# Kernel optimization log

Hardware: AMD Instinct MI355X
Metric: run time of the kernel (lower is better)

Reference implementation:

```python
import jax, jax.numpy as jnp
import numpy as np

D_MODEL = 1024
NUM_HEADS = 16
THETA = 10000.0
B, T = 2, 2048


def _rope(x, pos, theta_base):
    # x: (b, h, t, d_h); interleaved pairs (x0,x1),(x2,x3),... per the
    # rearrange '... (c d) -> ... c d' with d=2 in the original module.
    d = x.shape[-1]
    half = d // 2
    inv_freq = 1.0 / (theta_base ** (2.0 * jnp.arange(half, dtype=jnp.float32) / d))
    ang = pos.astype(jnp.float32)[:, None] * inv_freq[None, :]  # (t, half)
    sin = jnp.sin(ang)[None, None]  # (1,1,t,half)
    cos = jnp.cos(ang)[None, None]
    x1 = x[..., 0::2]
    x2 = x[..., 1::2]
    r1 = x1 * cos - x2 * sin
    r2 = x1 * sin + x2 * cos
    return jnp.stack([r1, r2], axis=-1).reshape(x.shape)


def setup_inputs() -> dict:
    key = jax.random.key(0)
    k0, k1, k2, k3, k4 = jax.random.split(key, 5)
    sigma = (2.0 / (D_MODEL + D_MODEL)) ** 0.5
    return {
        "in_features": jax.random.normal(k0, (B, T, D_MODEL), dtype=jnp.float32),
        "Wq": jax.random.normal(k1, (D_MODEL, D_MODEL), dtype=jnp.float32) * sigma,
        "Wk": jax.random.normal(k2, (D_MODEL, D_MODEL), dtype=jnp.float32) * sigma,
        "Wv": jax.random.normal(k3, (D_MODEL, D_MODEL), dtype=jnp.float32) * sigma,
        "Wo": jax.random.normal(k4, (D_MODEL, D_MODEL), dtype=jnp.float32) * sigma,
        "token_positions": jnp.arange(T, dtype=jnp.int32),
    }


def reference(in_features, Wq, Wk, Wv, Wo, token_positions):
    b, t, d_model = in_features.shape
    h = NUM_HEADS
    d_h = d_model // h
    # Fused-style QKV projections (x @ W.T, weights stored (in, out))
    q = in_features @ Wq.T
    k = in_features @ Wk.T
    v = in_features @ Wv.T
    # (b, t, h*d_h) -> (b, h, t, d_h)
    q = q.reshape(b, t, h, d_h).transpose(0, 2, 1, 3)
    k = k.reshape(b, t, h, d_h).transpose(0, 2, 1, 3)
    v = v.reshape(b, t, h, d_h).transpose(0, 2, 1, 3)
    q = _rope(q, token_positions, THETA)
    k = _rope(k, token_positions, THETA)
    scale = 1.0 / jnp.sqrt(jnp.asarray(d_h, dtype=q.dtype))
    scores = jnp.einsum('bhqd,bhkd->bhqk', q, k) * scale
    causal = jnp.tril(jnp.ones((t, t), dtype=bool))
    scores = jnp.where(causal[None, None], scores, -jnp.inf)
    attn = jax.nn.softmax(scores, axis=-1)
    out = jnp.einsum('bhqk,bhkd->bhqd', attn, v)
    out = out.transpose(0, 2, 1, 3).reshape(b, t, h * d_h)
    return out @ Wo.T
```

## Files before the change

kernel.cpp:

```cpp
#include <hip/hip_runtime.h>

#define D_MODEL 1024
#define NUM_HEADS 16
#define DH 64
#define B_SZ 2
#define T_SZ 2048
#define M_ROWS (B_SZ * T_SZ)

typedef __bf16 bf16;
typedef __bf16 bf16x4 __attribute__((ext_vector_type(4)));
typedef __bf16 bf16x8 __attribute__((ext_vector_type(8)));
typedef float f32x4 __attribute__((ext_vector_type(4)));

__device__ __forceinline__ void async_copy16(const bf16* g, bf16* l) {
  __builtin_amdgcn_global_load_lds(
      (const __attribute__((address_space(1))) void*)g,
      (__attribute__((address_space(3))) void*)l, 16, 0, 0);
}

#define NX (M_ROWS * D_MODEL / 4)
#define NW (D_MODEL * D_MODEL / 4)

__global__ __launch_bounds__(256) void cast_all(
    const float* __restrict__ X, const float* __restrict__ Wq,
    const float* __restrict__ Wk, const float* __restrict__ Wv,
    const float* __restrict__ Wo,
    bf16* __restrict__ Xb, bf16* __restrict__ Wqb, bf16* __restrict__ Wkb,
    bf16* __restrict__ Wvb, bf16* __restrict__ Wob) {
  int i = blockIdx.x * 256 + threadIdx.x;
  const float* s; bf16* d; int off;
  if (i < NX) {
    s = X; d = Xb; off = i;
  } else {
    int j = i - NX;
    int w = j >> 18;
    off = j & (NW - 1);
    if (w == 0)      { s = Wq; d = Wqb; }
    else if (w == 1) { s = Wk; d = Wkb; }
    else if (w == 2) { s = Wv; d = Wvb; }
    else             { s = Wo; d = Wob; }
  }
  float4 v = ((const float4*)s)[off];
  bf16x4 o;
  o[0] = (bf16)v.x; o[1] = (bf16)v.y; o[2] = (bf16)v.z; o[3] = (bf16)v.w;
  ((bf16x4*)d)[off] = o;
}

__global__ __launch_bounds__(256) void qkv_gemm(
    const bf16* __restrict__ Xb,
    const bf16* __restrict__ Wqb, const bf16* __restrict__ Wkb,
    const bf16* __restrict__ Wvb,
    bf16* __restrict__ Q, bf16* __restrict__ K, bf16* __restrict__ V) {
  __shared__ bf16 As[128 * 32];
  __shared__ bf16 Bs[128 * 32];

  int tid = threadIdx.x;
  int wave = tid >> 6, lane = tid & 63;
  int wm = wave >> 1, wn = wave & 1;
  int l15 = lane & 15, quad = lane >> 4;

  int row0 = blockIdx.x * 128;
  int col0 = blockIdx.y * 128;
  int sel = col0 >> 10;
  int nb = col0 & 1023;
  const bf16* W; bf16* Out;
  if (sel == 0)      { W = Wqb; Out = Q; }
  else if (sel == 1) { W = Wkb; Out = K; }
  else               { W = Wvb; Out = V; }

  int srow = tid >> 2;
  int schunk = tid & 3;
  const bf16* Ag = Xb + (size_t)(row0 + srow) * D_MODEL + schunk * 8;
  const bf16* Bg = W + (size_t)(nb + srow) * D_MODEL + schunk * 8;
  bf16* Al0 = &As[srow * 32 + schunk * 8];
  bf16* Al1 = &As[(srow + 64) * 32 + schunk * 8];
  bf16* Bl0 = &Bs[srow * 32 + schunk * 8];
  bf16* Bl1 = &Bs[(srow + 64) * 32 + schunk * 8];

  f32x4 acc[4][4];
#pragma unroll
  for (int i = 0; i < 4; ++i)
#pragma unroll
    for (int j = 0; j < 4; ++j) acc[i][j] = (f32x4){0.f, 0.f, 0.f, 0.f};

  for (int k0 = 0; k0 < D_MODEL; k0 += 32) {
    async_copy16(Ag + k0, Al0);
    async_copy16(Ag + k0 + (size_t)64 * D_MODEL, Al1);
    async_copy16(Bg + k0, Bl0);
    async_copy16(Bg + k0 + (size_t)64 * D_MODEL, Bl1);
    __syncthreads();

    bf16x8 af[4], bfr[4];
#pragma unroll
    for (int i = 0; i < 4; ++i)
      af[i] = *(const bf16x8*)&As[(wm * 64 + i * 16 + l15) * 32 + quad * 8];
#pragma unroll
    for (int j = 0; j < 4; ++j)
      bfr[j] = *(const bf16x8*)&Bs[(wn * 64 + j * 16 + l15) * 32 + quad * 8];
#pragma unroll
    for (int i = 0; i < 4; ++i)
#pragma unroll
      for (int j = 0; j < 4; ++j)
        acc[i][j] = __builtin_amdgcn_mfma_f32_16x16x32_bf16(af[i], bfr[j],
                                                            acc[i][j], 0, 0, 0);
    __syncthreads();
  }

#pragma unroll
  for (int i = 0; i < 4; ++i) {
    int row = row0 + wm * 64 + i * 16 + quad * 4;
#pragma unroll
    for (int j = 0; j < 4; ++j) {
      int col = nb + wn * 64 + j * 16 + l15;
#pragma unroll
      for (int r = 0; r < 4; ++r)
        Out[(size_t)(row + r) * D_MODEL + col] = (bf16)acc[i][j][r];
    }
  }
}

#define ROPEK_BLOCKS (M_ROWS * NUM_HEADS * 32 / 256)

__global__ __launch_bounds__(256) void ropek_vt(
    bf16* __restrict__ K, const bf16* __restrict__ V, bf16* __restrict__ VT,
    const int* __restrict__ pos) {
  int b0 = blockIdx.x;
  if (b0 < ROPEK_BLOCKS) {
    int idx = b0 * 256 + threadIdx.x;
    int i = idx & 31;
    int h = (idx >> 5) & 15;
    int row = idx >> 9;
    int t = row & (T_SZ - 1);
    float p = (float)pos[t];
    float freq = __expf(-(float)i * 0.28782313662425f);
    float s, c;
    sincosf(p * freq, &s, &c);
    size_t base = (size_t)row * D_MODEL + h * DH + 2 * i;
    float k1 = (float)K[base], k2 = (float)K[base + 1];
    K[base]     = (bf16)(k1 * c - k2 * s);
    K[base + 1] = (bf16)(k1 * s + k2 * c);
  } else {
    __shared__ bf16 tile[64][72];
    int vb = b0 - ROPEK_BLOCKS;
    int bh = vb >> 5;
    int tt = vb & 31;
    int b = bh >> 4, h = bh & 15;
    int tid = threadIdx.x;
    int rr = tid >> 3;
    int cc = (tid & 7) * 8;
#pragma unroll
    for (int p = 0; p < 2; ++p) {
      int t = rr + p * 32;
      bf16x8 v = *(const bf16x8*)&V[((size_t)b * T_SZ + tt * 64 + t) * D_MODEL +
                                    h * DH + cc];
      *(bf16x8*)&tile[t][cc] = v;
    }
    __syncthreads();
#pragma unroll
    for (int p = 0; p < 2; ++p) {
      int d = rr + p * 32;
      bf16x8 o;
#pragma unroll
      for (int j = 0; j < 8; ++j) o[j] = tile[cc + j][d];
      *(bf16x8*)&VT[((size_t)bh * DH + d) * T_SZ + tt * 64 + cc] = o;
    }
  }
}

#define PST 72

__global__ __launch_bounds__(512) void attn_kernel(
    const bf16* __restrict__ Q, const bf16* __restrict__ K,
    const bf16* __restrict__ VT, const int* __restrict__ pos,
    bf16* __restrict__ AO) {
  __shared__ bf16 Kt0[64 * 32], Kt1[64 * 32];
  __shared__ bf16 Vt0[64 * 32], Vt1[64 * 32];
  __shared__ bf16 Pbuf[8][16 * PST];

  int bh = blockIdx.x;
  int qi = 15 - (int)blockIdx.y;
  int bb = bh >> 4, h = bh & 15;
  int tid = threadIdx.x;
  int wave = tid >> 6, lane = tid & 63;
  int l15 = lane & 15, quad = lane >> 4;

  int q0 = qi * 128 + wave * 16;
  size_t grow = (size_t)bb * T_SZ + q0;

  const bf16* Qp = Q + (grow + l15) * D_MODEL + h * DH + quad * 8;
  bf16x8 bq0 = *(const bf16x8*)(Qp);
  bf16x8 bq1 = *(const bf16x8*)(Qp + 32);
  {
    float p = (float)pos[q0 + l15];
#pragma unroll
    for (int jj = 0; jj < 4; ++jj) {
      int i0 = quad * 4 + jj;
      float s, c;
      sincosf(p * __expf(-(float)i0 * 0.28782313662425f), &s, &c);
      float x1 = (float)bq0[2 * jj], x2 = (float)bq0[2 * jj + 1];
      bq0[2 * jj]     = (bf16)(x1 * c - x2 * s);
      bq0[2 * jj + 1] = (bf16)(x1 * s + x2 * c);
      sincosf(p * __expf(-(float)(i0 + 16) * 0.28782313662425f), &s, &c);
      float y1 = (float)bq1[2 * jj], y2 = (float)bq1[2 * jj + 1];
      bq1[2 * jj]     = (bf16)(y1 * c - y2 * s);
      bq1[2 * jj + 1] = (bf16)(y1 * s + y2 * c);
    }
  }

  f32x4 o[4];
#pragma unroll
  for (int nt = 0; nt < 4; ++nt) o[nt] = (f32x4){0.f, 0.f, 0.f, 0.f};
  float l_i = 0.f;

  bool isK = (tid < 256);
  int stid = isK ? tid : tid - 256;
  int srow = stid >> 2, sch = stid & 3;
  const bf16* sbase = isK
      ? K + ((size_t)bb * T_SZ + srow) * D_MODEL + h * DH + sch * 8
      : VT + ((size_t)bh * DH + srow) * T_SZ + sch * 8;
  size_t sstep = isK ? (size_t)64 * D_MODEL : (size_t)64;
  bf16* sdst0 = isK ? &Kt0[srow * 32 + sch * 8] : &Vt0[srow * 32 + sch * 8];
  bf16* sdst1 = isK ? &Kt1[srow * 32 + sch * 8] : &Vt1[srow * 32 + sch * 8];

  bf16* Pw = Pbuf[wave];
  int nchunks = 2 * qi + 2;
  int tb = 2 * qi + (wave >> 2);
  int bound = (wave & 3) * 16 + l15;

  for (int t = 0; t < nchunks; ++t) {
    const bf16* s = sbase + (size_t)t * sstep;
    async_copy16(s, sdst0);
    async_copy16(s + 32, sdst1);
    __syncthreads();

    if (t <= tb) {
      f32x4 st[4];
#pragma unroll
      for (int cs = 0; cs < 4; ++cs) {
        bf16x8 ak0 = *(const bf16x8*)&Kt0[(cs * 16 + l15) * 32 + quad * 8];
        bf16x8 ak1 = *(const bf16x8*)&Kt1[(cs * 16 + l15) * 32 + quad * 8];
        f32x4 s4 = (f32x4){0.f, 0.f, 0.f, 0.f};
        s4 = __builtin_amdgcn_mfma_f32_16x16x32_bf16(ak0, bq0, s4, 0, 0, 0);
        s4 = __builtin_amdgcn_mfma_f32_16x16x32_bf16(ak1, bq1, s4, 0, 0, 0);
        st[cs] = s4;
      }

      bool bm = (t == tb);
      float ps = 0.f;
#pragma unroll
      for (int cs = 0; cs < 4; ++cs)
#pragma unroll
        for (int r = 0; r < 4; ++r) {
          float p = __expf(st[cs][r] * 0.125f);
          if (bm) {
            int cl = cs * 16 + quad * 4 + r;
            p = (cl > bound) ? 0.f : p;
          }
          st[cs][r] = p;
          ps += p;
        }
      l_i += ps;

#pragma unroll
      for (int cs = 0; cs < 4; ++cs) {
        bf16x4 pk;
#pragma unroll
        for (int r = 0; r < 4; ++r) pk[r] = (bf16)st[cs][r];
        *(bf16x4*)&Pw[l15 * PST + cs * 16 + quad * 4] = pk;
      }
      __asm__ __volatile__("" ::: "memory");
      bf16x8 bp0 = *(const bf16x8*)&Pw[l15 * PST + quad * 8];
      bf16x8 bp1 = *(const bf16x8*)&Pw[l15 * PST + 32 + quad * 8];
      __asm__ __volatile__("" ::: "memory");

#pragma unroll
      for (int nt = 0; nt < 4; ++nt) {
        bf16x8 av0 = *(const bf16x8*)&Vt0[(nt * 16 + l15) * 32 + quad * 8];
        bf16x8 av1 = *(const bf16x8*)&Vt1[(nt * 16 + l15) * 32 + quad * 8];
        o[nt] = __builtin_amdgcn_mfma_f32_16x16x32_bf16(av0, bp0, o[nt], 0, 0, 0);
        o[nt] = __builtin_amdgcn_mfma_f32_16x16x32_bf16(av1, bp1, o[nt], 0, 0, 0);
      }
    }
    __syncthreads();
  }

  l_i += __shfl_xor(l_i, 16);
  l_i += __shfl_xor(l_i, 32);
  float inv = 1.0f / l_i;
#pragma unroll
  for (int nt = 0; nt < 4; ++nt) {
    bf16x4 ov;
#pragma unroll
    for (int r = 0; r < 4; ++r) ov[r] = (bf16)(o[nt][r] * inv);
    *(bf16x4*)&AO[(grow + l15) * D_MODEL + h * DH + nt * 16 + quad * 4] = ov;
  }
}

__global__ __launch_bounds__(256) void out_gemm(
    const bf16* __restrict__ AO, const bf16* __restrict__ Wob,
    float* __restrict__ out) {
  __shared__ bf16 As[128 * 32];
  __shared__ bf16 Bs[128 * 32];

  int tid = threadIdx.x;
  int wave = tid >> 6, lane = tid & 63;
  int wm = wave >> 1, wn = wave & 1;
  int l15 = lane & 15, quad = lane >> 4;

  int row0 = blockIdx.x * 128;
  int nb = blockIdx.y * 128;

  int srow = tid >> 2;
  int schunk = tid & 3;
  const bf16* Ag = AO + (size_t)(row0 + srow) * D_MODEL + schunk * 8;
  const bf16* Bg = Wob + (size_t)(nb + srow) * D_MODEL + schunk * 8;
  bf16* Al0 = &As[srow * 32 + schunk * 8];
  bf16* Al1 = &As[(srow + 64) * 32 + schunk * 8];
  bf16* Bl0 = &Bs[srow * 32 + schunk * 8];
  bf16* Bl1 = &Bs[(srow + 64) * 32 + schunk * 8];

  f32x4 acc[4][4];
#pragma unroll
  for (int i = 0; i < 4; ++i)
#pragma unroll
    for (int j = 0; j < 4; ++j) acc[i][j] = (f32x4){0.f, 0.f, 0.f, 0.f};

  for (int k0 = 0; k0 < D_MODEL; k0 += 32) {
    async_copy16(Ag + k0, Al0);
    async_copy16(Ag + k0 + (size_t)64 * D_MODEL, Al1);
    async_copy16(Bg + k0, Bl0);
    async_copy16(Bg + k0 + (size_t)64 * D_MODEL, Bl1);
    __syncthreads();

    bf16x8 af[4], bfr[4];
#pragma unroll
    for (int i = 0; i < 4; ++i)
      af[i] = *(const bf16x8*)&As[(wm * 64 + i * 16 + l15) * 32 + quad * 8];
#pragma unroll
    for (int j = 0; j < 4; ++j)
      bfr[j] = *(const bf16x8*)&Bs[(wn * 64 + j * 16 + l15) * 32 + quad * 8];
#pragma unroll
    for (int i = 0; i < 4; ++i)
#pragma unroll
      for (int j = 0; j < 4; ++j)
        acc[i][j] = __builtin_amdgcn_mfma_f32_16x16x32_bf16(af[i], bfr[j],
                                                            acc[i][j], 0, 0, 0);
    __syncthreads();
  }

#pragma unroll
  for (int i = 0; i < 4; ++i) {
    int row = row0 + wm * 64 + i * 16 + quad * 4;
#pragma unroll
    for (int j = 0; j < 4; ++j) {
      int col = nb + wn * 64 + j * 16 + l15;
#pragma unroll
      for (int r = 0; r < 4; ++r)
        out[(size_t)(row + r) * D_MODEL + col] = acc[i][j][r];
    }
  }
}

extern "C" void kernel_launch(void* const* d_in, const int* in_sizes, int n_in,
                              void* d_out, int out_size, void* d_ws, size_t ws_size,
                              hipStream_t stream) {
  const float* X  = (const float*)d_in[0];
  const float* Wq = (const float*)d_in[1];
  const float* Wk = (const float*)d_in[2];
  const float* Wv = (const float*)d_in[3];
  const float* Wo = (const float*)d_in[4];
  const int*  pos = (const int*)d_in[5];
  float* out = (float*)d_out;

  char* w = (char*)d_ws;
  bf16* Xb  = (bf16*)w;  w += (size_t)M_ROWS * D_MODEL * 2;
  bf16* Wqb = (bf16*)w;  w += (size_t)D_MODEL * D_MODEL * 2;
  bf16* Wkb = (bf16*)w;  w += (size_t)D_MODEL * D_MODEL * 2;
  bf16* Wvb = (bf16*)w;  w += (size_t)D_MODEL * D_MODEL * 2;
  bf16* Wob = (bf16*)w;  w += (size_t)D_MODEL * D_MODEL * 2;
  bf16* Qb  = (bf16*)w;  w += (size_t)M_ROWS * D_MODEL * 2;
  bf16* Kb  = (bf16*)w;  w += (size_t)M_ROWS * D_MODEL * 2;
  bf16* Vb  = (bf16*)w;  w += (size_t)M_ROWS * D_MODEL * 2;
  bf16* AO  = (bf16*)w;  w += (size_t)M_ROWS * D_MODEL * 2;
  bf16* VT  = (bf16*)w;  w += (size_t)M_ROWS * D_MODEL * 2;

  cast_all<<<(NX + 4 * NW) / 256, 256, 0, stream>>>(X, Wq, Wk, Wv, Wo,
                                                    Xb, Wqb, Wkb, Wvb, Wob);
  qkv_gemm<<<dim3(M_ROWS / 128, 3 * D_MODEL / 128), 256, 0, stream>>>(
      Xb, Wqb, Wkb, Wvb, Qb, Kb, Vb);
  ropek_vt<<<ROPEK_BLOCKS + B_SZ * NUM_HEADS * (T_SZ / 64), 256, 0, stream>>>(
      Kb, Vb, VT, pos);
  attn_kernel<<<dim3(B_SZ * NUM_HEADS, T_SZ / 128), 512, 0, stream>>>(
      Qb, Kb, VT, pos, AO);
  out_gemm<<<dim3(M_ROWS / 128, D_MODEL / 128), 256, 0, stream>>>(AO, Wob, out);
}
```

Before: 196.1 us.

## Shrink attention query tiles, prefetch K/V via registers, halve out_gemm N tile

The attention kernel moves from 128-query blocks with 512 threads to 64-query blocks with 256 threads. This doubles the grid and removes the idle waves that skipped the final causal chunk. K/V staging changes from async global-to-LDS copies into a register prefetch of the next chunk, stored into padded LDS tiles (stride 72) to reduce bank conflicts. The output GEMM tile drops to 128x64 so more blocks launch. The trade-off is more K/V reloading per query and lower MFMA reuse per block in the output GEMM.

```diff
diff --git a/kernel.cpp b/kernel.cpp
--- a/kernel.cpp
+++ b/kernel.cpp
@@ -168,23 +168,24 @@
 }
 
 #define PST 72
-
-__global__ __launch_bounds__(512) void attn_kernel(
+#define KST 72
+
+__global__ __launch_bounds__(256) void attn_kernel(
     const bf16* __restrict__ Q, const bf16* __restrict__ K,
     const bf16* __restrict__ VT, const int* __restrict__ pos,
     bf16* __restrict__ AO) {
-  __shared__ bf16 Kt0[64 * 32], Kt1[64 * 32];
-  __shared__ bf16 Vt0[64 * 32], Vt1[64 * 32];
-  __shared__ bf16 Pbuf[8][16 * PST];
+  __shared__ bf16 Kt[64 * KST];
+  __shared__ bf16 Vt[64 * KST];
+  __shared__ bf16 Pbuf[4][16 * PST];
 
   int bh = blockIdx.x;
-  int qi = 15 - (int)blockIdx.y;
+  int qi = 31 - (int)blockIdx.y;
   int bb = bh >> 4, h = bh & 15;
   int tid = threadIdx.x;
   int wave = tid >> 6, lane = tid & 63;
   int l15 = lane & 15, quad = lane >> 4;
 
-  int q0 = qi * 128 + wave * 16;
+  int q0 = qi * 64 + wave * 16;
   size_t grow = (size_t)bb * T_SZ + q0;
 
   const bf16* Qp = Q + (grow + l15) * D_MODEL + h * DH + quad * 8;
@@ -212,76 +213,84 @@
   for (int nt = 0; nt < 4; ++nt) o[nt] = (f32x4){0.f, 0.f, 0.f, 0.f};
   float l_i = 0.f;
 
-  bool isK = (tid < 256);
-  int stid = isK ? tid : tid - 256;
-  int srow = stid >> 2, sch = stid & 3;
-  const bf16* sbase = isK
-      ? K + ((size_t)bb * T_SZ + srow) * D_MODEL + h * DH + sch * 8
-      : VT + ((size_t)bh * DH + srow) * T_SZ + sch * 8;
-  size_t sstep = isK ? (size_t)64 * D_MODEL : (size_t)64;
-  bf16* sdst0 = isK ? &Kt0[srow * 32 + sch * 8] : &Vt0[srow * 32 + sch * 8];
-  bf16* sdst1 = isK ? &Kt1[srow * 32 + sch * 8] : &Vt1[srow * 32 + sch * 8];
+  int srow = tid >> 2;
+  int sc = (tid & 3) * 16;
+  const bf16* Kg = K + ((size_t)bb * T_SZ + srow) * D_MODEL + h * DH + sc;
+  const bf16* Vg = VT + ((size_t)bh * DH + srow) * T_SZ + sc;
+  bf16* Kl = &Kt[srow * KST + sc];
+  bf16* Vl = &Vt[srow * KST + sc];
 
   bf16* Pw = Pbuf[wave];
-  int nchunks = 2 * qi + 2;
-  int tb = 2 * qi + (wave >> 2);
-  int bound = (wave & 3) * 16 + l15;
+  int nchunks = qi + 1;
+  int rel = wave * 16 + l15;
+
+  bf16x8 kr0 = *(const bf16x8*)(Kg);
+  bf16x8 kr1 = *(const bf16x8*)(Kg + 8);
+  bf16x8 vr0 = *(const bf16x8*)(Vg);
+  bf16x8 vr1 = *(const bf16x8*)(Vg + 8);
 
   for (int t = 0; t < nchunks; ++t) {
-    const bf16* s = sbase + (size_t)t * sstep;
-    async_copy16(s, sdst0);
-    async_copy16(s + 32, sdst1);
-    __syncthreads();
-
-    if (t <= tb) {
-      f32x4 st[4];
-#pragma unroll
-      for (int cs = 0; cs < 4; ++cs) {
-        bf16x8 ak0 = *(const bf16x8*)&Kt0[(cs * 16 + l15) * 32 + quad * 8];
-        bf16x8 ak1 = *(const bf16x8*)&Kt1[(cs * 16 + l15) * 32 + quad * 8];
-        f32x4 s4 = (f32x4){0.f, 0.f, 0.f, 0.f};
-        s4 = __builtin_amdgcn_mfma_f32_16x16x32_bf16(ak0, bq0, s4, 0, 0, 0);
-        s4 = __builtin_amdgcn_mfma_f32_16x16x32_bf16(ak1, bq1, s4, 0, 0, 0);
-        st[cs] = s4;
+    __syncthreads();
+    *(bf16x8*)(Kl) = kr0;
+    *(bf16x8*)(Kl + 8) = kr1;
+    *(bf16x8*)(Vl) = vr0;
+    *(bf16x8*)(Vl + 8) = vr1;
+    if (t + 1 < nchunks) {
+      const bf16* Kn = Kg + (size_t)(t + 1) * 64 * D_MODEL;
+      const bf16* Vn = Vg + (t + 1) * 64;
+      kr0 = *(const bf16x8*)(Kn);
+      kr1 = *(const bf16x8*)(Kn + 8);
+      vr0 = *(const bf16x8*)(Vn);
+      vr1 = *(const bf16x8*)(Vn + 8);
+    }
+    __syncthreads();
+
+    f32x4 st[4];
+#pragma unroll
+    for (int cs = 0; cs < 4; ++cs) {
+      bf16x8 ak0 = *(const bf16x8*)&Kt[(cs * 16 + l15) * KST + quad * 8];
+      bf16x8 ak1 = *(const bf16x8*)&Kt[(cs * 16 + l15) * KST + 32 + quad * 8];
+      f32x4 s4 = (f32x4){0.f, 0.f, 0.f, 0.f};
+      s4 = __builtin_amdgcn_mfma_f32_16x16x32_bf16(ak0, bq0, s4, 0, 0, 0);
+      s4 = __builtin_amdgcn_mfma_f32_16x16x32_bf16(ak1, bq1, s4, 0, 0, 0);
+      st[cs] = s4;
+    }
+
+    bool last = (t == nchunks - 1);
+    float ps = 0.f;
+#pragma unroll
+    for (int cs = 0; cs < 4; ++cs)
+#pragma unroll
+      for (int r = 0; r < 4; ++r) {
+        float p = __expf(st[cs][r] * 0.125f);
+        if (last) {
+          int cl = cs * 16 + quad * 4 + r;
+          p = (cl > rel) ? 0.f : p;
+        }
+        st[cs][r] = p;
+        ps += p;
       }
-
-      bool bm = (t == tb);
-      float ps = 0.f;
-#pragma unroll
-      for (int cs = 0; cs < 4; ++cs)
-#pragma unroll
-        for (int r = 0; r < 4; ++r) {
-          float p = __expf(st[cs][r] * 0.125f);
-          if (bm) {
-            int cl = cs * 16 + quad * 4 + r;
-            p = (cl > bound) ? 0.f : p;
-          }
-          st[cs][r] = p;
-          ps += p;
-        }
-      l_i += ps;
-
-#pragma unroll
-      for (int cs = 0; cs < 4; ++cs) {
-        bf16x4 pk;
-#pragma unroll
-        for (int r = 0; r < 4; ++r) pk[r] = (bf16)st[cs][r];
-        *(bf16x4*)&Pw[l15 * PST + cs * 16 + quad * 4] = pk;
-      }
-      __asm__ __volatile__("" ::: "memory");
-      bf16x8 bp0 = *(const bf16x8*)&Pw[l15 * PST + quad * 8];
-      bf16x8 bp1 = *(const bf16x8*)&Pw[l15 * PST + 32 + quad * 8];
-      __asm__ __volatile__("" ::: "memory");
-
-#pragma unroll
-      for (int nt = 0; nt < 4; ++nt) {
-        bf16x8 av0 = *(const bf16x8*)&Vt0[(nt * 16 + l15) * 32 + quad * 8];
-        bf16x8 av1 = *(const bf16x8*)&Vt1[(nt * 16 + l15) * 32 + quad * 8];
-        o[nt] = __builtin_amdgcn_mfma_f32_16x16x32_bf16(av0, bp0, o[nt], 0, 0, 0);
-        o[nt] = __builtin_amdgcn_mfma_f32_16x16x32_bf16(av1, bp1, o[nt], 0, 0, 0);
-      }
-    }
-    __syncthreads();
+    l_i += ps;
+
+#pragma unroll
+    for (int cs = 0; cs < 4; ++cs) {
+      bf16x4 pk;
+#pragma unroll
+      for (int r = 0; r < 4; ++r) pk[r] = (bf16)st[cs][r];
+      *(bf16x4*)&Pw[l15 * PST + cs * 16 + quad * 4] = pk;
+    }
+    __asm__ __volatile__("" ::: "memory");
+    bf16x8 bp0 = *(const bf16x8*)&Pw[l15 * PST + quad * 8];
+    bf16x8 bp1 = *(const bf16x8*)&Pw[l15 * PST + 32 + quad * 8];
+    __asm__ __volatile__("" ::: "memory");
+
+#pragma unroll
+    for (int nt = 0; nt < 4; ++nt) {
+      bf16x8 av0 = *(const bf16x8*)&Vt[(nt * 16 + l15) * KST + quad * 8];
+      bf16x8 av1 = *(const bf16x8*)&Vt[(nt * 16 + l15) * KST + 32 + quad * 8];
+      o[nt] = __builtin_amdgcn_mfma_f32_16x16x32_bf16(av0, bp0, o[nt], 0, 0, 0);
+      o[nt] = __builtin_amdgcn_mfma_f32_16x16x32_bf16(av1, bp1, o[nt], 0, 0, 0);
+    }
   }
 
   l_i += __shfl_xor(l_i, 16);
@@ -300,15 +309,14 @@
     const bf16* __restrict__ AO, const bf16* __restrict__ Wob,
     float* __restrict__ out) {
   __shared__ bf16 As[128 * 32];
-  __shared__ bf16 Bs[128 * 32];
+  __shared__ bf16 Bs[64 * 32];
 
   int tid = threadIdx.x;
   int wave = tid >> 6, lane = tid & 63;
-  int wm = wave >> 1, wn = wave & 1;
   int l15 = lane & 15, quad = lane >> 4;
 
   int row0 = blockIdx.x * 128;
-  int nb = blockIdx.y * 128;
+  int nb = blockIdx.y * 64;
 
   int srow = tid >> 2;
   int schunk = tid & 3;
@@ -316,31 +324,29 @@
   const bf16* Bg = Wob + (size_t)(nb + srow) * D_MODEL + schunk * 8;
   bf16* Al0 = &As[srow * 32 + schunk * 8];
   bf16* Al1 = &As[(srow + 64) * 32 + schunk * 8];
-  bf16* Bl0 = &Bs[srow * 32 + schunk * 8];
-  bf16* Bl1 = &Bs[(srow + 64) * 32 + schunk * 8];
-
-  f32x4 acc[4][4];
-#pragma unroll
-  for (int i = 0; i < 4; ++i)
+  bf16* Bl = &Bs[srow * 32 + schunk * 8];
+
+  f32x4 acc[2][4];
+#pragma unroll
+  for (int i = 0; i < 2; ++i)
 #pragma unroll
     for (int j = 0; j < 4; ++j) acc[i][j] = (f32x4){0.f, 0.f, 0.f, 0.f};
 
   for (int k0 = 0; k0 < D_MODEL; k0 += 32) {
     async_copy16(Ag + k0, Al0);
     async_copy16(Ag + k0 + (size_t)64 * D_MODEL, Al1);
-    async_copy16(Bg + k0, Bl0);
-    async_copy16(Bg + k0 + (size_t)64 * D_MODEL, Bl1);
-    __syncthreads();
-
-    bf16x8 af[4], bfr[4];
-#pragma unroll
-    for (int i = 0; i < 4; ++i)
-      af[i] = *(const bf16x8*)&As[(wm * 64 + i * 16 + l15) * 32 + quad * 8];
+    async_copy16(Bg + k0, Bl);
+    __syncthreads();
+
+    bf16x8 af[2], bfr[4];
+#pragma unroll
+    for (int i = 0; i < 2; ++i)
+      af[i] = *(const bf16x8*)&As[(wave * 32 + i * 16 + l15) * 32 + quad * 8];
 #pragma unroll
     for (int j = 0; j < 4; ++j)
-      bfr[j] = *(const bf16x8*)&Bs[(wn * 64 + j * 16 + l15) * 32 + quad * 8];
-#pragma unroll
-    for (int i = 0; i < 4; ++i)
+      bfr[j] = *(const bf16x8*)&Bs[(j * 16 + l15) * 32 + quad * 8];
+#pragma unroll
+    for (int i = 0; i < 2; ++i)
 #pragma unroll
       for (int j = 0; j < 4; ++j)
         acc[i][j] = __builtin_amdgcn_mfma_f32_16x16x32_bf16(af[i], bfr[j],
@@ -349,11 +355,11 @@
   }
 
 #pragma unroll
-  for (int i = 0; i < 4; ++i) {
-    int row = row0 + wm * 64 + i * 16 + quad * 4;
+  for (int i = 0; i < 2; ++i) {
+    int row = row0 + wave * 32 + i * 16 + quad * 4;
 #pragma unroll
     for (int j = 0; j < 4; ++j) {
-      int col = nb + wn * 64 + j * 16 + l15;
+      int col = nb + j * 16 + l15;
 #pragma unroll
       for (int r = 0; r < 4; ++r)
         out[(size_t)(row + r) * D_MODEL + col] = acc[i][j][r];
@@ -390,7 +396,7 @@
       Xb, Wqb, Wkb, Wvb, Qb, Kb, Vb);
   ropek_vt<<<ROPEK_BLOCKS + B_SZ * NUM_HEADS * (T_SZ / 64), 256, 0, stream>>>(
       Kb, Vb, VT, pos);
-  attn_kernel<<<dim3(B_SZ * NUM_HEADS, T_SZ / 128), 512, 0, stream>>>(
+  attn_kernel<<<dim3(B_SZ * NUM_HEADS, T_SZ / 64), 256, 0, stream>>>(
       Qb, Kb, VT, pos, AO);
-  out_gemm<<<dim3(M_ROWS / 128, D_MODEL / 128), 256, 0, stream>>>(AO, Wob, out);
-}
+  out_gemm<<<dim3(M_ROWS / 128, D_MODEL / 64), 256, 0, stream>>>(AO, Wob, out);
+}
```

New measurement: 185.6 us. -5.4%, faster.
